# Kernel tuning notes

Hardware: AMD Instinct MI355X
Metric: run time of the kernel (lower is better)

The kernel has to match this reference:

```python
import jax, jax.numpy as jnp
import numpy as np

B, Mc, Mt, E, VOCAB, NREL, HOPS = 16, 2048, 4096, 512, 32000, 69, 2


def setup_inputs() -> dict:
    key = jax.random.key(0)
    ks = jax.random.split(key, 10)
    s = 1.0 / np.sqrt(E)
    return {
        "concept_table": jax.random.normal(ks[0], (VOCAB, E), jnp.float32) * 0.02,
        "relation_table": jax.random.normal(ks[1], (NREL, E), jnp.float32) * 0.02,
        "W_s": jax.random.uniform(ks[2], (HOPS, E, E), jnp.float32, -s, s),
        "W_n": jax.random.uniform(ks[3], (HOPS, E, E), jnp.float32, -s, s),
        "W_r": jax.random.uniform(ks[4], (HOPS, E, E), jnp.float32, -s, s),
        "concept_ids": jax.random.randint(ks[5], (B, Mc), 0, VOCAB, jnp.int32),
        "relation_ids": jax.random.randint(ks[6], (B, Mt), 0, NREL, jnp.int32),
        "head_idx": jax.random.randint(ks[7], (B, Mt), 0, Mc, jnp.int32),
        "tail_idx": jax.random.randint(ks[8], (B, Mt), 0, Mc, jnp.int32),
        "triple_labels": jax.random.randint(ks[9], (B, Mt), -1, 2, jnp.int32),
    }


def reference(concept_table, relation_table, W_s, W_n, W_r,
              concept_ids, relation_ids, head_idx, tail_idx, triple_labels):
    b, mt = head_idx.shape
    mc = concept_ids.shape[1]
    h = concept_table[concept_ids]          # B x Mc x E
    r = relation_table[relation_ids]        # B x Mt x E
    valid = (triple_labels != -1)
    mask = valid[..., None].astype(h.dtype)  # B x Mt x 1
    cnt = valid.astype(h.dtype)              # B x Mt
    bidx = jnp.arange(b)[:, None]
    num_hops = W_s.shape[0]
    for l in range(num_hops):
        rm = r * mask
        o_h = jnp.take_along_axis(h, head_idx[..., None], axis=1) * mask
        o_t = jnp.take_along_axis(h, tail_idx[..., None], axis=1) * mask
        upd = jnp.zeros_like(h)
        upd = upd.at[bidx, tail_idx].add(o_h - rm)   # messages head->tail
        upd = upd.at[bidx, head_idx].add(o_t - rm)   # messages tail->head
        count = jnp.zeros((b, mc), h.dtype)
        count = count.at[bidx, tail_idx].add(cnt).at[bidx, head_idx].add(cnt)
        h = jax.nn.relu(h @ W_s[l].T + (upd @ W_n[l].T) / jnp.clip(count, 1.0)[..., None])
        r = r @ W_r[l].T
    head_repr = jnp.take_along_axis(h, head_idx[..., None], axis=1)  # B x Mt x E
    tail_repr = jnp.take_along_axis(h, tail_idx[..., None], axis=1)
    return jnp.concatenate((head_repr, r, tail_repr), axis=-1)       # B x Mt x 3E
```

## Files before the change

### kernel.cpp

```cpp
#include <hip/hip_runtime.h>
#include <stdint.h>

#define B_   16
#define MC   2048
#define MT   4096
#define E_   512
#define NRELS 69

typedef __attribute__((ext_vector_type(8))) short bf16x8;
typedef __attribute__((ext_vector_type(4))) float floatx4;

__device__ inline float b2f(ushort u) {
  union { uint32_t i; float f; } x; x.i = ((uint32_t)u) << 16; return x.f;
}
__device__ inline ushort f2b(float f) {
  union { float f; uint32_t u; } v; v.f = f;
  uint32_t r = (v.u + 0x7fffu + ((v.u >> 16) & 1u)) >> 16;
  return (ushort)r;
}

__global__ void detect_k(const ushort* __restrict__ t, int* __restrict__ flag) {
  int bad = 0;
  for (int j = threadIdx.x; j < 4096; j += 256) {
    int e = (t[j] >> 7) & 0xFF;
    if (e >= 0xC0) bad = 1;
  }
  if (bad) atomicOr(flag, 1);
}

__global__ void cvt_k(const void* __restrict__ src, ushort* __restrict__ dst, int n8,
                      const int* __restrict__ flag) {
  int c = blockIdx.x * blockDim.x + threadIdx.x;
  if (c >= n8) return;
  if (*flag) {
    const float* s = (const float*)src + (size_t)c * 8;
    float4 a = *(const float4*)s, b = *(const float4*)(s + 4);
    uint32_t p0 = (uint32_t)f2b(a.x) | ((uint32_t)f2b(a.y) << 16);
    uint32_t p1 = (uint32_t)f2b(a.z) | ((uint32_t)f2b(a.w) << 16);
    uint32_t p2 = (uint32_t)f2b(b.x) | ((uint32_t)f2b(b.y) << 16);
    uint32_t p3 = (uint32_t)f2b(b.z) | ((uint32_t)f2b(b.w) << 16);
    *(uint4*)(dst + (size_t)c * 8) = make_uint4(p0, p1, p2, p3);
  } else {
    *(uint4*)(dst + (size_t)c * 8) = *(const uint4*)((const ushort*)src + (size_t)c * 8);
  }
}

__global__ void gather_h_k(const void* __restrict__ table, const int* __restrict__ ids,
                           ushort* __restrict__ out, int nrows, const int* __restrict__ flag) {
  int c = blockIdx.x * blockDim.x + threadIdx.x;
  int row = c >> 6;
  if (row >= nrows) return;
  int col = (c & 63) << 3;
  int src = ids[row];
  if (*flag) {
    const float* s = (const float*)table + (size_t)src * E_ + col;
    float4 a = *(const float4*)s, b = *(const float4*)(s + 4);
    uint32_t p0 = (uint32_t)f2b(a.x) | ((uint32_t)f2b(a.y) << 16);
    uint32_t p1 = (uint32_t)f2b(a.z) | ((uint32_t)f2b(a.w) << 16);
    uint32_t p2 = (uint32_t)f2b(b.x) | ((uint32_t)f2b(b.y) << 16);
    uint32_t p3 = (uint32_t)f2b(b.z) | ((uint32_t)f2b(b.w) << 16);
    *(uint4*)(out + (size_t)row * E_ + col) = make_uint4(p0, p1, p2, p3);
  } else {
    *(uint4*)(out + (size_t)row * E_ + col) =
        *(const uint4*)((const ushort*)table + (size_t)src * E_ + col);
  }
}

__global__ void count_k(const int* __restrict__ head, const int* __restrict__ tail,
                        const int* __restrict__ labels, int* __restrict__ cnt) {
  int t = blockIdx.x * blockDim.x + threadIdx.x;
  if (t >= B_ * MT) return;
  if (labels[t] == -1) return;
  int b = t >> 12;
  atomicAdd(&cnt[b * MC + head[t]], 1);
  atomicAdd(&cnt[b * MC + tail[t]], 1);
}

__global__ void inv_k(const int* __restrict__ cnt, float* __restrict__ inv, int n) {
  int i = blockIdx.x * blockDim.x + threadIdx.x;
  if (i < n) {
    int c = cnt[i];
    inv[i] = 1.0f / (float)(c > 1 ? c : 1);
  }
}

__global__ void scan_k(const int* __restrict__ cnt, int* __restrict__ offs) {
  __shared__ int part[256];
  int tid = threadIdx.x;
  const int CH = (B_ * MC) / 256;
  int base = tid * CH, s = 0;
  for (int i = 0; i < CH; ++i) s += cnt[base + i];
  part[tid] = s;
  __syncthreads();
  for (int off = 1; off < 256; off <<= 1) {
    int v = (tid >= off) ? part[tid - off] : 0;
    __syncthreads();
    part[tid] += v;
    __syncthreads();
  }
  int run = (tid == 0) ? 0 : part[tid - 1];
  for (int i = 0; i < CH; ++i) { offs[base + i] = run; run += cnt[base + i]; }
  if (tid == 255) offs[B_ * MC] = run;
}

__global__ void fill_k(const int* __restrict__ head, const int* __restrict__ tail,
                       const int* __restrict__ rid, const int* __restrict__ labels,
                       const int* __restrict__ offs, int* __restrict__ cursor,
                       int* __restrict__ edges) {
  int t = blockIdx.x * blockDim.x + threadIdx.x;
  if (t >= B_ * MT) return;
  if (labels[t] == -1) return;
  int b = t >> 12;
  int hb = b * MC + head[t], tb = b * MC + tail[t];
  int r = rid[t];
  int p = atomicAdd(&cursor[tb], 1);
  edges[offs[tb] + p] = head[t] | (r << 16);
  p = atomicAdd(&cursor[hb], 1);
  edges[offs[hb] + p] = tail[t] | (r << 16);
}

__global__ void gather_msg_k(const ushort* __restrict__ h, const ushort* __restrict__ rtab,
                             const int* __restrict__ edges, const int* __restrict__ offs,
                             const float* __restrict__ inv, ushort* __restrict__ updb) {
  int row = blockIdx.x * 4 + (threadIdx.x >> 6);
  int lane = threadIdx.x & 63;
  int col = lane << 3;
  int beg = offs[row], end = offs[row + 1];
  int b = row >> 11;
  float acc[8];
#pragma unroll
  for (int i = 0; i < 8; ++i) acc[i] = 0.f;
  const ushort* hbase = h + (size_t)b * MC * E_ + col;
  for (int e = beg; e < end; ++e) {
    int ent = edges[e];
    int other = ent & 0xffff, rid = ent >> 16;
    uint4 vh = *(const uint4*)(hbase + (size_t)other * E_);
    uint4 vr = *(const uint4*)(rtab + (size_t)rid * E_ + col);
    uint32_t wh[4] = {vh.x, vh.y, vh.z, vh.w};
    uint32_t wr[4] = {vr.x, vr.y, vr.z, vr.w};
#pragma unroll
    for (int i = 0; i < 4; ++i) {
      acc[2 * i]     += b2f((ushort)(wh[i] & 0xffff)) - b2f((ushort)(wr[i] & 0xffff));
      acc[2 * i + 1] += b2f((ushort)(wh[i] >> 16))    - b2f((ushort)(wr[i] >> 16));
    }
  }
  float s = inv[row];
  uint32_t p[4];
#pragma unroll
  for (int i = 0; i < 4; ++i)
    p[i] = (uint32_t)f2b(acc[2 * i] * s) | ((uint32_t)f2b(acc[2 * i + 1] * s) << 16);
  *(uint4*)(updb + (size_t)row * E_ + col) = make_uint4(p[0], p[1], p[2], p[3]);
}

__global__ void rel_gemm_k(const ushort* __restrict__ in, const ushort* __restrict__ W,
                           ushort* __restrict__ outt) {
  __shared__ float arow[E_];
  int n = blockIdx.x;
  int tid = threadIdx.x;
  for (int k = tid; k < E_; k += 256) arow[k] = b2f(in[n * E_ + k]);
  __syncthreads();
#pragma unroll
  for (int c0 = 0; c0 < E_; c0 += 256) {
    int c = c0 + tid;
    float acc = 0.f;
    const ushort* wr = W + (size_t)c * E_;
    for (int k = 0; k < E_; k += 8) {
      uint4 w8 = *(const uint4*)(wr + k);
      uint32_t ww[4] = {w8.x, w8.y, w8.z, w8.w};
#pragma unroll
      for (int i = 0; i < 4; ++i) {
        acc += arow[k + 2 * i]     * b2f((ushort)(ww[i] & 0xffff));
        acc += arow[k + 2 * i + 1] * b2f((ushort)(ww[i] >> 16));
      }
    }
    outt[n * E_ + c] = f2b(acc);
  }
}

#define BM 128
#define BN 128
#define BK 64
#define BKP 72

__global__ __launch_bounds__(256) void gemm_h_k(
    const ushort* __restrict__ A0, const ushort* __restrict__ W0,
    const ushort* __restrict__ A1, const ushort* __restrict__ W1,
    ushort* __restrict__ C) {
  const int N = E_, K = E_;
  __shared__ ushort As[BM * BKP];
  __shared__ ushort Bs[BN * BKP];
  int nbn = N / BN;
  int bm = blockIdx.x / nbn, bn = blockIdx.x % nbn;
  int tid = threadIdx.x;
  int lane = tid & 63, wid = tid >> 6;
  int wm = (wid >> 1) * 64, wn = (wid & 1) * 64;
  int lrow = lane & 15, lq = lane >> 4;

  floatx4 acc[4][4];
#pragma unroll
  for (int i = 0; i < 4; ++i)
#pragma unroll
    for (int j = 0; j < 4; ++j) acc[i][j] = (floatx4)(0.0f);

  for (int pass = 0; pass < 2; ++pass) {
    const ushort* Am = pass ? A1 : A0;
    const ushort* Wm = pass ? W1 : W0;
    for (int k0 = 0; k0 < K; k0 += BK) {
#pragma unroll
      for (int i = 0; i < 4; ++i) {
        int c = tid + i * 256;
        int row = c >> 3, col = (c & 7) << 3;
        *(uint4*)(As + row * BKP + col) =
            *(const uint4*)(Am + (size_t)(bm * BM + row) * K + k0 + col);
      }
#pragma unroll
      for (int i = 0; i < 4; ++i) {
        int c = tid + i * 256;
        int row = c >> 3, col = (c & 7) << 3;
        *(uint4*)(Bs + row * BKP + col) =
            *(const uint4*)(Wm + (size_t)(bn * BN + row) * K + k0 + col);
      }
      __syncthreads();
#pragma unroll
      for (int kk = 0; kk < BK; kk += 32) {
        bf16x8 af[4], bfr[4];
#pragma unroll
        for (int mi = 0; mi < 4; ++mi)
          af[mi] = *(const bf16x8*)(As + (wm + mi * 16 + lrow) * BKP + kk + lq * 8);
#pragma unroll
        for (int ni = 0; ni < 4; ++ni)
          bfr[ni] = *(const bf16x8*)(Bs + (wn + ni * 16 + lrow) * BKP + kk + lq * 8);
#pragma unroll
        for (int mi = 0; mi < 4; ++mi)
#pragma unroll
          for (int ni = 0; ni < 4; ++ni)
            acc[mi][ni] = __builtin_amdgcn_mfma_f32_16x16x32_bf16(af[mi], bfr[ni], acc[mi][ni], 0, 0, 0);
      }
      __syncthreads();
    }
  }
#pragma unroll
  for (int mi = 0; mi < 4; ++mi)
#pragma unroll
    for (int ni = 0; ni < 4; ++ni)
#pragma unroll
      for (int rg = 0; rg < 4; ++rg) {
        int row = bm * BM + wm + mi * 16 + lq * 4 + rg;
        int col = bn * BN + wn + ni * 16 + lrow;
        C[(size_t)row * N + col] = f2b(fmaxf(acc[mi][ni][rg], 0.0f));
      }
}

__global__ void out_k(const ushort* __restrict__ h, const ushort* __restrict__ rtab,
                      const int* __restrict__ rid,
                      const int* __restrict__ head, const int* __restrict__ tail,
                      void* __restrict__ out, const int* __restrict__ flag) {
  int gid = blockIdx.x * blockDim.x + threadIdx.x;
  int t = gid / 192;
  if (t >= B_ * MT) return;
  int sc = gid - t * 192;
  int sec = sc >> 6;
  int col = (sc & 63) << 3;
  int b = t >> 12;
  const ushort* src;
  if (sec == 0)      src = h + (size_t)(b * MC + head[t]) * E_ + col;
  else if (sec == 1) src = rtab + (size_t)rid[t] * E_ + col;
  else               src = h + (size_t)(b * MC + tail[t]) * E_ + col;
  size_t o = (size_t)t * 1536 + sec * 512 + col;
  if (*flag) {
    float* fo = (float*)out + o;
    uint4 v = *(const uint4*)src;
    uint32_t w[4] = {v.x, v.y, v.z, v.w};
    float4 f0, f1;
    f0.x = b2f((ushort)(w[0] & 0xffff)); f0.y = b2f((ushort)(w[0] >> 16));
    f0.z = b2f((ushort)(w[1] & 0xffff)); f0.w = b2f((ushort)(w[1] >> 16));
    f1.x = b2f((ushort)(w[2] & 0xffff)); f1.y = b2f((ushort)(w[2] >> 16));
    f1.z = b2f((ushort)(w[3] & 0xffff)); f1.w = b2f((ushort)(w[3] >> 16));
    *(float4*)fo = f0;
    *(float4*)(fo + 4) = f1;
  } else {
    *(uint4*)((ushort*)out + o) = *(const uint4*)src;
  }
}

extern "C" void kernel_launch(void* const* d_in, const int* in_sizes, int n_in,
                              void* d_out, int out_size, void* d_ws, size_t ws_size,
                              hipStream_t stream) {
  const void* concept_table  = d_in[0];
  const void* relation_table = d_in[1];
  const void* W_s = d_in[2];
  const void* W_n = d_in[3];
  const void* W_r = d_in[4];
  const int* concept_ids  = (const int*)d_in[5];
  const int* relation_ids = (const int*)d_in[6];
  const int* head_idx = (const int*)d_in[7];
  const int* tail_idx = (const int*)d_in[8];
  const int* labels   = (const int*)d_in[9];

  char* ws = (char*)d_ws;
  size_t off = 0;
  auto alloc = [&](size_t bytes) {
    char* p = ws + off;
    off += (bytes + 255) & ~(size_t)255;
    return p;
  };
  int*    flag   = (int*)   alloc(256);
  ushort* h_a    = (ushort*)alloc((size_t)B_ * MC * E_ * 2);
  ushort* h_b    = (ushort*)alloc((size_t)B_ * MC * E_ * 2);
  int*    cnt    = (int*)   alloc((size_t)B_ * MC * 4);
  float*  inv    = (float*) alloc((size_t)B_ * MC * 4);
  int*    offs   = (int*)   alloc(((size_t)B_ * MC + 1) * 4);
  int*    cursor = (int*)   alloc((size_t)B_ * MC * 4);
  int*    edges  = (int*)   alloc((size_t)2 * B_ * MT * 4);
  ushort* Wsb    = (ushort*)alloc((size_t)2 * E_ * E_ * 2);
  ushort* Wnb    = (ushort*)alloc((size_t)2 * E_ * E_ * 2);
  ushort* Wrb    = (ushort*)alloc((size_t)2 * E_ * E_ * 2);
  ushort* rtab0  = (ushort*)alloc((size_t)NRELS * E_ * 2);
  ushort* rtab1  = (ushort*)alloc((size_t)NRELS * E_ * 2);
  ushort* rtab2  = (ushort*)alloc((size_t)NRELS * E_ * 2);
  ushort* updb   = (ushort*)d_out;

  hipMemsetAsync(flag, 0, 4, stream);
  detect_k<<<1, 256, 0, stream>>>((const ushort*)concept_table, flag);

  int nw8 = 2 * E_ * E_ / 8;
  cvt_k<<<(nw8 + 255) / 256, 256, 0, stream>>>(W_s, Wsb, nw8, flag);
  cvt_k<<<(nw8 + 255) / 256, 256, 0, stream>>>(W_n, Wnb, nw8, flag);
  cvt_k<<<(nw8 + 255) / 256, 256, 0, stream>>>(W_r, Wrb, nw8, flag);
  int nr8 = NRELS * E_ / 8;
  cvt_k<<<(nr8 + 255) / 256, 256, 0, stream>>>(relation_table, rtab0, nr8, flag);

  gather_h_k<<<(B_ * MC * 64 + 255) / 256, 256, 0, stream>>>(concept_table, concept_ids, h_a,
                                                             B_ * MC, flag);

  hipMemsetAsync(cnt, 0, (size_t)B_ * MC * 4, stream);
  count_k<<<(B_ * MT + 255) / 256, 256, 0, stream>>>(head_idx, tail_idx, labels, cnt);
  inv_k<<<(B_ * MC + 255) / 256, 256, 0, stream>>>(cnt, inv, B_ * MC);
  scan_k<<<1, 256, 0, stream>>>(cnt, offs);
  hipMemsetAsync(cursor, 0, (size_t)B_ * MC * 4, stream);
  fill_k<<<(B_ * MT + 255) / 256, 256, 0, stream>>>(head_idx, tail_idx, relation_ids, labels,
                                                    offs, cursor, edges);

  rel_gemm_k<<<NRELS, 256, 0, stream>>>(rtab0, Wrb, rtab1);
  rel_gemm_k<<<NRELS, 256, 0, stream>>>(rtab1, Wrb + (size_t)E_ * E_, rtab2);

  gather_msg_k<<<B_ * MC / 4, 256, 0, stream>>>(h_a, rtab0, edges, offs, inv, updb);
  gemm_h_k<<<(B_ * MC / BM) * (E_ / BN), 256, 0, stream>>>(h_a, Wsb, updb, Wnb, h_b);

  gather_msg_k<<<B_ * MC / 4, 256, 0, stream>>>(h_b, rtab1, edges, offs, inv, updb);
  gemm_h_k<<<(B_ * MC / BM) * (E_ / BN), 256, 0, stream>>>(h_b, Wsb + (size_t)E_ * E_, updb,
                                                           Wnb + (size_t)E_ * E_, h_a);

  out_k<<<(B_ * MT * 192 + 255) / 256, 256, 0, stream>>>(h_a, rtab2, relation_ids,
                                                         head_idx, tail_idx, d_out, flag);
}
```

Baseline: 713.7 us.

## Fuse preprocessing kernels, merge relation GEMMs, and use direct global-to-LDS loads

Collapses the detect, convert, gather and count kernels into one preprocessing launch, with each block redoing a small dtype-detection check in place of a global flag. Scan and inverse-count computation are merged into one 1024-thread kernel, and the two relation-table GEMMs are chained inside one kernel. The main hidden-state GEMM now uses global_load_lds to stage tiles directly into unpadded LDS. This is meant to cut launch and memset overhead and register staging, at the risk of LDS bank conflicts from dropping the padding and redundant per-block detection reads.

```diff
diff --git a/kernel.cpp b/kernel.cpp
--- a/kernel.cpp
+++ b/kernel.cpp
@@ -10,6 +10,9 @@
 typedef __attribute__((ext_vector_type(8))) short bf16x8;
 typedef __attribute__((ext_vector_type(4))) float floatx4;
 
+typedef __attribute__((address_space(1))) const void gvoid_t;
+typedef __attribute__((address_space(3))) void lvoid_t;
+
 __device__ inline float b2f(ushort u) {
   union { uint32_t i; float f; } x; x.i = ((uint32_t)u) << 16; return x.f;
 }
@@ -19,20 +22,26 @@
   return (ushort)r;
 }
 
-__global__ void detect_k(const ushort* __restrict__ t, int* __restrict__ flag) {
+__device__ inline void gl2lds(const ushort* g, ushort* l) {
+  __builtin_amdgcn_global_load_lds((gvoid_t*)g, (lvoid_t*)l, 16, 0, 0);
+}
+
+__device__ inline int block_detect(const ushort* ct) {
+  __shared__ int sflag;
+  if (threadIdx.x == 0) sflag = 0;
+  __syncthreads();
   int bad = 0;
-  for (int j = threadIdx.x; j < 4096; j += 256) {
-    int e = (t[j] >> 7) & 0xFF;
+  for (int j = threadIdx.x; j < 1024; j += 256) {
+    int e = (ct[j] >> 7) & 0xFF;
     if (e >= 0xC0) bad = 1;
   }
-  if (bad) atomicOr(flag, 1);
-}
-
-__global__ void cvt_k(const void* __restrict__ src, ushort* __restrict__ dst, int n8,
-                      const int* __restrict__ flag) {
-  int c = blockIdx.x * blockDim.x + threadIdx.x;
-  if (c >= n8) return;
-  if (*flag) {
+  if (bad) sflag = 1;
+  __syncthreads();
+  return sflag;
+}
+
+__device__ inline void cvt8(const void* src, ushort* dst, int c, int flag) {
+  if (flag) {
     const float* s = (const float*)src + (size_t)c * 8;
     float4 a = *(const float4*)s, b = *(const float4*)(s + 4);
     uint32_t p0 = (uint32_t)f2b(a.x) | ((uint32_t)f2b(a.y) << 16);
@@ -45,62 +54,83 @@
   }
 }
 
-__global__ void gather_h_k(const void* __restrict__ table, const int* __restrict__ ids,
-                           ushort* __restrict__ out, int nrows, const int* __restrict__ flag) {
-  int c = blockIdx.x * blockDim.x + threadIdx.x;
-  int row = c >> 6;
-  if (row >= nrows) return;
-  int col = (c & 63) << 3;
-  int src = ids[row];
-  if (*flag) {
-    const float* s = (const float*)table + (size_t)src * E_ + col;
-    float4 a = *(const float4*)s, b = *(const float4*)(s + 4);
-    uint32_t p0 = (uint32_t)f2b(a.x) | ((uint32_t)f2b(a.y) << 16);
-    uint32_t p1 = (uint32_t)f2b(a.z) | ((uint32_t)f2b(a.w) << 16);
-    uint32_t p2 = (uint32_t)f2b(b.x) | ((uint32_t)f2b(b.y) << 16);
-    uint32_t p3 = (uint32_t)f2b(b.z) | ((uint32_t)f2b(b.w) << 16);
-    *(uint4*)(out + (size_t)row * E_ + col) = make_uint4(p0, p1, p2, p3);
+#define NW8 (2 * E_ * E_ / 8)
+#define NR8 (NRELS * E_ / 8)
+#define NGH (B_ * MC * 64)
+#define NCT (B_ * MT)
+#define SEC1 (NW8)
+#define SEC2 (2 * NW8)
+#define SEC3 (3 * NW8)
+#define SEC4 (SEC3 + NR8)
+#define SEC5 (SEC4 + NGH)
+#define STOT (SEC5 + NCT)
+
+__global__ void preproc_k(const void* __restrict__ ct, const void* __restrict__ rt,
+                          const void* __restrict__ Ws, const void* __restrict__ Wn,
+                          const void* __restrict__ Wr,
+                          const int* __restrict__ cids, const int* __restrict__ heads,
+                          const int* __restrict__ tails, const int* __restrict__ labels,
+                          ushort* __restrict__ Wsb, ushort* __restrict__ Wnb,
+                          ushort* __restrict__ Wrb, ushort* __restrict__ rtab0,
+                          ushort* __restrict__ h0, int* __restrict__ cnt) {
+  int flag = block_detect((const ushort*)ct);
+  int c = blockIdx.x * 256 + threadIdx.x;
+  if (c >= STOT) return;
+  if (c < SEC3) {
+    if (c < SEC1)       cvt8(Ws, Wsb, c, flag);
+    else if (c < SEC2)  cvt8(Wn, Wnb, c - SEC1, flag);
+    else                cvt8(Wr, Wrb, c - SEC2, flag);
+  } else if (c < SEC4) {
+    cvt8(rt, rtab0, c - SEC3, flag);
+  } else if (c < SEC5) {
+    int g = c - SEC4;
+    int row = g >> 6, col = (g & 63) << 3;
+    int src = cids[row];
+    if (flag) {
+      const float* s = (const float*)ct + (size_t)src * E_ + col;
+      float4 a = *(const float4*)s, b = *(const float4*)(s + 4);
+      uint32_t p0 = (uint32_t)f2b(a.x) | ((uint32_t)f2b(a.y) << 16);
+      uint32_t p1 = (uint32_t)f2b(a.z) | ((uint32_t)f2b(a.w) << 16);
+      uint32_t p2 = (uint32_t)f2b(b.x) | ((uint32_t)f2b(b.y) << 16);
+      uint32_t p3 = (uint32_t)f2b(b.z) | ((uint32_t)f2b(b.w) << 16);
+      *(uint4*)(h0 + (size_t)row * E_ + col) = make_uint4(p0, p1, p2, p3);
+    } else {
+      *(uint4*)(h0 + (size_t)row * E_ + col) =
+          *(const uint4*)((const ushort*)ct + (size_t)src * E_ + col);
+    }
   } else {
-    *(uint4*)(out + (size_t)row * E_ + col) =
-        *(const uint4*)((const ushort*)table + (size_t)src * E_ + col);
-  }
-}
-
-__global__ void count_k(const int* __restrict__ head, const int* __restrict__ tail,
-                        const int* __restrict__ labels, int* __restrict__ cnt) {
-  int t = blockIdx.x * blockDim.x + threadIdx.x;
-  if (t >= B_ * MT) return;
-  if (labels[t] == -1) return;
-  int b = t >> 12;
-  atomicAdd(&cnt[b * MC + head[t]], 1);
-  atomicAdd(&cnt[b * MC + tail[t]], 1);
-}
-
-__global__ void inv_k(const int* __restrict__ cnt, float* __restrict__ inv, int n) {
-  int i = blockIdx.x * blockDim.x + threadIdx.x;
-  if (i < n) {
-    int c = cnt[i];
-    inv[i] = 1.0f / (float)(c > 1 ? c : 1);
-  }
-}
-
-__global__ void scan_k(const int* __restrict__ cnt, int* __restrict__ offs) {
-  __shared__ int part[256];
+    int t = c - SEC5;
+    if (labels[t] != -1) {
+      int b = t >> 12;
+      atomicAdd(&cnt[b * MC + heads[t]], 1);
+      atomicAdd(&cnt[b * MC + tails[t]], 1);
+    }
+  }
+}
+
+__global__ void scan_inv_k(const int* __restrict__ cnt, int* __restrict__ offs,
+                           float* __restrict__ inv) {
+  __shared__ int part[1024];
   int tid = threadIdx.x;
-  const int CH = (B_ * MC) / 256;
+  const int CH = (B_ * MC) / 1024;
   int base = tid * CH, s = 0;
   for (int i = 0; i < CH; ++i) s += cnt[base + i];
   part[tid] = s;
   __syncthreads();
-  for (int off = 1; off < 256; off <<= 1) {
+  for (int off = 1; off < 1024; off <<= 1) {
     int v = (tid >= off) ? part[tid - off] : 0;
     __syncthreads();
     part[tid] += v;
     __syncthreads();
   }
   int run = (tid == 0) ? 0 : part[tid - 1];
-  for (int i = 0; i < CH; ++i) { offs[base + i] = run; run += cnt[base + i]; }
-  if (tid == 255) offs[B_ * MC] = run;
+  for (int i = 0; i < CH; ++i) {
+    int cc = cnt[base + i];
+    offs[base + i] = run;
+    inv[base + i] = 1.0f / (float)(cc > 1 ? cc : 1);
+    run += cc;
+  }
+  if (tid == 1023) offs[B_ * MC] = run;
 }
 
 __global__ void fill_k(const int* __restrict__ head, const int* __restrict__ tail,
@@ -152,43 +182,53 @@
   *(uint4*)(updb + (size_t)row * E_ + col) = make_uint4(p[0], p[1], p[2], p[3]);
 }
 
-__global__ void rel_gemm_k(const ushort* __restrict__ in, const ushort* __restrict__ W,
-                           ushort* __restrict__ outt) {
+__global__ void rel2_gemm_k(const ushort* __restrict__ rtab0, const ushort* __restrict__ Wr,
+                            ushort* __restrict__ rtab1, ushort* __restrict__ rtab2) {
   __shared__ float arow[E_];
   int n = blockIdx.x;
   int tid = threadIdx.x;
-  for (int k = tid; k < E_; k += 256) arow[k] = b2f(in[n * E_ + k]);
+  for (int k = tid; k < E_; k += 256) arow[k] = b2f(rtab0[n * E_ + k]);
   __syncthreads();
-#pragma unroll
-  for (int c0 = 0; c0 < E_; c0 += 256) {
-    int c = c0 + tid;
-    float acc = 0.f;
-    const ushort* wr = W + (size_t)c * E_;
+  for (int hp = 0; hp < 2; ++hp) {
+    const ushort* W = Wr + (size_t)hp * E_ * E_;
+    int ca = tid, cb = tid + 256;
+    float acc0 = 0.f, acc1 = 0.f;
+    const ushort* wa = W + (size_t)ca * E_;
+    const ushort* wb = W + (size_t)cb * E_;
     for (int k = 0; k < E_; k += 8) {
-      uint4 w8 = *(const uint4*)(wr + k);
-      uint32_t ww[4] = {w8.x, w8.y, w8.z, w8.w};
+      uint4 w8a = *(const uint4*)(wa + k);
+      uint4 w8b = *(const uint4*)(wb + k);
+      uint32_t va[4] = {w8a.x, w8a.y, w8a.z, w8a.w};
+      uint32_t vb[4] = {w8b.x, w8b.y, w8b.z, w8b.w};
 #pragma unroll
       for (int i = 0; i < 4; ++i) {
-        acc += arow[k + 2 * i]     * b2f((ushort)(ww[i] & 0xffff));
-        acc += arow[k + 2 * i + 1] * b2f((ushort)(ww[i] >> 16));
-      }
-    }
-    outt[n * E_ + c] = f2b(acc);
+        float a0 = arow[k + 2 * i], a1 = arow[k + 2 * i + 1];
+        acc0 += a0 * b2f((ushort)(va[i] & 0xffff)) + a1 * b2f((ushort)(va[i] >> 16));
+        acc1 += a0 * b2f((ushort)(vb[i] & 0xffff)) + a1 * b2f((ushort)(vb[i] >> 16));
+      }
+    }
+    __syncthreads();
+    ushort ra = f2b(acc0), rb = f2b(acc1);
+    ushort* o = hp ? rtab2 : rtab1;
+    o[n * E_ + ca] = ra;
+    o[n * E_ + cb] = rb;
+    arow[ca] = b2f(ra);
+    arow[cb] = b2f(rb);
+    __syncthreads();
   }
 }
 
 #define BM 128
 #define BN 128
 #define BK 64
-#define BKP 72
 
 __global__ __launch_bounds__(256) void gemm_h_k(
     const ushort* __restrict__ A0, const ushort* __restrict__ W0,
     const ushort* __restrict__ A1, const ushort* __restrict__ W1,
     ushort* __restrict__ C) {
   const int N = E_, K = E_;
-  __shared__ ushort As[BM * BKP];
-  __shared__ ushort Bs[BN * BKP];
+  __shared__ __align__(16) ushort As[BM * BK];
+  __shared__ __align__(16) ushort Bs[BN * BK];
   int nbn = N / BN;
   int bm = blockIdx.x / nbn, bn = blockIdx.x % nbn;
   int tid = threadIdx.x;
@@ -210,15 +250,13 @@
       for (int i = 0; i < 4; ++i) {
         int c = tid + i * 256;
         int row = c >> 3, col = (c & 7) << 3;
-        *(uint4*)(As + row * BKP + col) =
-            *(const uint4*)(Am + (size_t)(bm * BM + row) * K + k0 + col);
+        gl2lds(Am + (size_t)(bm * BM + row) * K + k0 + col, As + row * BK + col);
       }
 #pragma unroll
       for (int i = 0; i < 4; ++i) {
         int c = tid + i * 256;
         int row = c >> 3, col = (c & 7) << 3;
-        *(uint4*)(Bs + row * BKP + col) =
-            *(const uint4*)(Wm + (size_t)(bn * BN + row) * K + k0 + col);
+        gl2lds(Wm + (size_t)(bn * BN + row) * K + k0 + col, Bs + row * BK + col);
       }
       __syncthreads();
 #pragma unroll
@@ -226,10 +264,10 @@
         bf16x8 af[4], bfr[4];
 #pragma unroll
         for (int mi = 0; mi < 4; ++mi)
-          af[mi] = *(const bf16x8*)(As + (wm + mi * 16 + lrow) * BKP + kk + lq * 8);
+          af[mi] = *(const bf16x8*)(As + (wm + mi * 16 + lrow) * BK + kk + lq * 8);
 #pragma unroll
         for (int ni = 0; ni < 4; ++ni)
-          bfr[ni] = *(const bf16x8*)(Bs + (wn + ni * 16 + lrow) * BKP + kk + lq * 8);
+          bfr[ni] = *(const bf16x8*)(Bs + (wn + ni * 16 + lrow) * BK + kk + lq * 8);
 #pragma unroll
         for (int mi = 0; mi < 4; ++mi)
 #pragma unroll
@@ -254,7 +292,8 @@
 __global__ void out_k(const ushort* __restrict__ h, const ushort* __restrict__ rtab,
                       const int* __restrict__ rid,
                       const int* __restrict__ head, const int* __restrict__ tail,
-                      void* __restrict__ out, const int* __restrict__ flag) {
+                      void* __restrict__ out, const ushort* __restrict__ ctab) {
+  int flag = block_detect(ctab);
   int gid = blockIdx.x * blockDim.x + threadIdx.x;
   int t = gid / 192;
   if (t >= B_ * MT) return;
@@ -267,7 +306,7 @@
   else if (sec == 1) src = rtab + (size_t)rid[t] * E_ + col;
   else               src = h + (size_t)(b * MC + tail[t]) * E_ + col;
   size_t o = (size_t)t * 1536 + sec * 512 + col;
-  if (*flag) {
+  if (flag) {
     float* fo = (float*)out + o;
     uint4 v = *(const uint4*)src;
     uint32_t w[4] = {v.x, v.y, v.z, v.w};
@@ -304,7 +343,6 @@
     off += (bytes + 255) & ~(size_t)255;
     return p;
   };
-  int*    flag   = (int*)   alloc(256);
   ushort* h_a    = (ushort*)alloc((size_t)B_ * MC * E_ * 2);
   ushort* h_b    = (ushort*)alloc((size_t)B_ * MC * E_ * 2);
   int*    cnt    = (int*)   alloc((size_t)B_ * MC * 4);
@@ -320,29 +358,19 @@
   ushort* rtab2  = (ushort*)alloc((size_t)NRELS * E_ * 2);
   ushort* updb   = (ushort*)d_out;
 
-  hipMemsetAsync(flag, 0, 4, stream);
-  detect_k<<<1, 256, 0, stream>>>((const ushort*)concept_table, flag);
-
-  int nw8 = 2 * E_ * E_ / 8;
-  cvt_k<<<(nw8 + 255) / 256, 256, 0, stream>>>(W_s, Wsb, nw8, flag);
-  cvt_k<<<(nw8 + 255) / 256, 256, 0, stream>>>(W_n, Wnb, nw8, flag);
-  cvt_k<<<(nw8 + 255) / 256, 256, 0, stream>>>(W_r, Wrb, nw8, flag);
-  int nr8 = NRELS * E_ / 8;
-  cvt_k<<<(nr8 + 255) / 256, 256, 0, stream>>>(relation_table, rtab0, nr8, flag);
-
-  gather_h_k<<<(B_ * MC * 64 + 255) / 256, 256, 0, stream>>>(concept_table, concept_ids, h_a,
-                                                             B_ * MC, flag);
-
   hipMemsetAsync(cnt, 0, (size_t)B_ * MC * 4, stream);
-  count_k<<<(B_ * MT + 255) / 256, 256, 0, stream>>>(head_idx, tail_idx, labels, cnt);
-  inv_k<<<(B_ * MC + 255) / 256, 256, 0, stream>>>(cnt, inv, B_ * MC);
-  scan_k<<<1, 256, 0, stream>>>(cnt, offs);
   hipMemsetAsync(cursor, 0, (size_t)B_ * MC * 4, stream);
+
+  preproc_k<<<(STOT + 255) / 256, 256, 0, stream>>>(
+      concept_table, relation_table, W_s, W_n, W_r,
+      concept_ids, head_idx, tail_idx, labels,
+      Wsb, Wnb, Wrb, rtab0, h_a, cnt);
+
+  scan_inv_k<<<1, 1024, 0, stream>>>(cnt, offs, inv);
   fill_k<<<(B_ * MT + 255) / 256, 256, 0, stream>>>(head_idx, tail_idx, relation_ids, labels,
                                                     offs, cursor, edges);
 
-  rel_gemm_k<<<NRELS, 256, 0, stream>>>(rtab0, Wrb, rtab1);
-  rel_gemm_k<<<NRELS, 256, 0, stream>>>(rtab1, Wrb + (size_t)E_ * E_, rtab2);
+  rel2_gemm_k<<<NRELS, 256, 0, stream>>>(rtab0, Wrb, rtab1, rtab2);
 
   gather_msg_k<<<B_ * MC / 4, 256, 0, stream>>>(h_a, rtab0, edges, offs, inv, updb);
   gemm_h_k<<<(B_ * MC / BM) * (E_ / BN), 256, 0, stream>>>(h_a, Wsb, updb, Wnb, h_b);
@@ -352,5 +380,6 @@
                                                            Wnb + (size_t)E_ * E_, h_a);
 
   out_k<<<(B_ * MT * 192 + 255) / 256, 256, 0, stream>>>(h_a, rtab2, relation_ids,
-                                                         head_idx, tail_idx, d_out, flag);
-}
+                                                         head_idx, tail_idx, d_out,
+                                                         (const ushort*)concept_table);
+}
```

Measured after the change: 718.4 us. Within noise of the previous version (+0.7%).
